# Kernel tuning notes

Measured on AMD Instinct MI355X. Metric: run time of the kernel, lower is better.

Reference implementation:

```python
import jax, jax.numpy as jnp
import numpy as np

B_SZ, LATENT, HIDDEN, T_STEPS = 512, 256, 512, 8
RTOL, ATOL = 1e-3, 1e-4
MAX_STEPS = 12          # adaptive sub-steps per output segment
SAFETY, MIN_FAC, MAX_FAC = 0.9, 0.2, 10.0

# Dormand-Prince 5(4) Butcher tableau (same as torchdiffeq's dopri5)
_C = [0.0, 0.2, 0.3, 0.8, 8.0 / 9.0, 1.0, 1.0]
_A = [
    [],
    [0.2],
    [3 / 40, 9 / 40],
    [44 / 45, -56 / 15, 32 / 9],
    [19372 / 6561, -25360 / 2187, 64448 / 6561, -212 / 729],
    [9017 / 3168, -355 / 33, 46732 / 5247, 49 / 176, -5103 / 18656],
    [35 / 384, 0.0, 500 / 1113, 125 / 192, -2187 / 6784, 11 / 84],
]
_B5 = [35 / 384, 0.0, 500 / 1113, 125 / 192, -2187 / 6784, 11 / 84, 0.0]
_B4 = [5179 / 57600, 0.0, 7571 / 16695, 393 / 640, -92097 / 339200, 187 / 2100, 1 / 40]


def _ode_rhs(p, t, z):
    # dz/dt = MLP([z, t]); t is a traced scalar
    b = z.shape[0]
    zt = jnp.concatenate([z, jnp.broadcast_to(t, (b, 1)).astype(z.dtype)], axis=1)
    h = jax.nn.relu(zt @ p['W1'] + p['b1'])
    h = jax.nn.relu(h @ p['W2'] + p['b2'])
    h = jax.nn.relu(h @ p['W3'] + p['b3'])
    return h @ p['W4'] + p['b4']


def _dopri5_step(p, t, z, dt):
    ks = []
    for i in range(7):
        zi = z
        for j, aij in enumerate(_A[i]):
            if aij != 0.0:
                zi = zi + (dt * aij) * ks[j]
        ks.append(_ode_rhs(p, t + _C[i] * dt, zi))
    z5 = z
    err = jnp.zeros_like(z)
    for i in range(7):
        if _B5[i] != 0.0:
            z5 = z5 + (dt * _B5[i]) * ks[i]
        d = _B5[i] - _B4[i]
        if d != 0.0:
            err = err + (dt * d) * ks[i]
    return z5, err


def _integrate(p, z0, t_grid):
    # adaptive dopri5 from t_grid[0] to each subsequent time, bounded work via scan
    def segment(carry, ts):
        z, dt = carry
        t0, t1 = ts[0], ts[1]

        def step(c, _):
            z, t, dt = c
            remaining = t1 - t
            active = remaining > 1e-10
            dt_try = jnp.minimum(dt, remaining)
            z5, err = _dopri5_step(p, t, z, dt_try)
            scale = ATOL + RTOL * jnp.maximum(jnp.abs(z), jnp.abs(z5))
            err_norm = jnp.sqrt(jnp.mean((err / scale) ** 2))
            accept = err_norm <= 1.0
            factor = jnp.clip(SAFETY * jnp.maximum(err_norm, 1e-9) ** -0.2, MIN_FAC, MAX_FAC)
            ok = jnp.logical_and(active, accept)
            z_n = jnp.where(ok, z5, z)
            t_n = jnp.where(ok, t + dt_try, t)
            dt_n = jnp.where(active, dt_try * factor, dt)
            return (z_n, t_n, dt_n), None

        (z, _, dt), _ = jax.lax.scan(step, (z, t0, dt), None, length=MAX_STEPS)
        return (z, dt), z

    dt0 = (t_grid[1] - t_grid[0]) * 0.1
    segs = jnp.stack([t_grid[:-1], t_grid[1:]], axis=1)  # [T-1, 2]
    (_, _), z_rest = jax.lax.scan(segment, (z0, dt0), segs)
    return jnp.concatenate([z0[None], z_rest], axis=0)  # [T, B, D]


def _pose_head(p, z):
    # z: [B, T, D]; dropout is identity in eval mode
    h = jax.nn.relu(z @ p['P1'] + p['pb1'])
    h = jax.nn.relu(h @ p['P2'] + p['pb2'])
    h = jax.nn.relu(h @ p['P3'] + p['pb3'])
    pose = h @ p['P4'] + p['pb4']  # [B, T, 7]
    pos, quat = pose[..., :3], pose[..., 3:]
    quat = quat / jnp.maximum(jnp.linalg.norm(quat, axis=-1, keepdims=True), 1e-12)
    return jnp.concatenate([pos, quat], axis=-1)


def setup_inputs() -> dict:
    key = jax.random.key(0)
    ks = jax.random.split(key, 12)
    n = jax.random.normal
    return {
        'z0': n(ks[0], (B_SZ, LATENT), dtype=jnp.float32),
        'time_steps': jnp.arange(T_STEPS, dtype=jnp.float32) / (T_STEPS - 1),
        # ODEFunc params (init std 0.1, zero bias per source)
        'W1': 0.1 * n(ks[1], (LATENT + 1, HIDDEN), dtype=jnp.float32),
        'b1': jnp.zeros((HIDDEN,), jnp.float32),
        'W2': 0.1 * n(ks[2], (HIDDEN, HIDDEN), dtype=jnp.float32),
        'b2': jnp.zeros((HIDDEN,), jnp.float32),
        'W3': 0.1 * n(ks[3], (HIDDEN, HIDDEN), dtype=jnp.float32),
        'b3': jnp.zeros((HIDDEN,), jnp.float32),
        'W4': 0.1 * n(ks[4], (HIDDEN, LATENT), dtype=jnp.float32),
        'b4': jnp.zeros((LATENT,), jnp.float32),
        # Pose head params
        'P1': 0.0625 * n(ks[5], (LATENT, 512), dtype=jnp.float32),
        'pb1': jnp.zeros((512,), jnp.float32),
        'P2': 0.0442 * n(ks[6], (512, 256), dtype=jnp.float32),
        'pb2': jnp.zeros((256,), jnp.float32),
        'P3': 0.0625 * n(ks[7], (256, 128), dtype=jnp.float32),
        'pb3': jnp.zeros((128,), jnp.float32),
        'P4': 0.01 * n(ks[8], (128, 7), dtype=jnp.float32),
        'pb4': jnp.zeros((7,), jnp.float32),
    }


def reference(z0, time_steps, W1, b1, W2, b2, W3, b3, W4, b4,
              P1, pb1, P2, pb2, P3, pb3, P4, pb4):
    p = dict(W1=W1, b1=b1, W2=W2, b2=b2, W3=W3, b3=b3, W4=W4, b4=b4,
             P1=P1, pb1=pb1, P2=P2, pb2=pb2, P3=P3, pb3=pb3, P4=P4, pb4=pb4)
    z_traj = _integrate(p, z0, time_steps)          # [T, B, D]
    z_traj = jnp.transpose(z_traj, (1, 0, 2))        # [B, T, D]
    poses = _pose_head(p, z_traj)                    # [B, T, 7]
    return poses
```

## Files before the change

### kernel.cpp

```cpp
#include <hip/hip_runtime.h>
#include <hip/hip_bf16.h>
#include <hip/hip_fp16.h>
#include <hip/hip_cooperative_groups.h>

namespace cg = cooperative_groups;

typedef unsigned short us16;
typedef unsigned int uu32;
typedef _Float16 h2v __attribute__((ext_vector_type(2)));

__constant__ float c_A[7][6] = {
  {0.f,0.f,0.f,0.f,0.f,0.f},
  {0.2f,0.f,0.f,0.f,0.f,0.f},
  {(float)(3.0/40.0),(float)(9.0/40.0),0.f,0.f,0.f,0.f},
  {(float)(44.0/45.0),(float)(-56.0/15.0),(float)(32.0/9.0),0.f,0.f,0.f},
  {(float)(19372.0/6561.0),(float)(-25360.0/2187.0),(float)(64448.0/6561.0),(float)(-212.0/729.0),0.f,0.f},
  {(float)(9017.0/3168.0),(float)(-355.0/33.0),(float)(46732.0/5247.0),(float)(49.0/176.0),(float)(-5103.0/18656.0),0.f},
  {(float)(35.0/384.0),0.f,(float)(500.0/1113.0),(float)(125.0/192.0),(float)(-2187.0/6784.0),(float)(11.0/84.0)}
};
__constant__ float c_C[7]  = {0.f,0.2f,0.3f,0.8f,(float)(8.0/9.0),1.f,1.f};
__constant__ float c_B5[7] = {(float)(35.0/384.0),0.f,(float)(500.0/1113.0),(float)(125.0/192.0),
                              (float)(-2187.0/6784.0),(float)(11.0/84.0),0.f};
__constant__ float c_D[7]  = {
  (float)(35.0/384.0 - 5179.0/57600.0), 0.f,
  (float)(500.0/1113.0 - 7571.0/16695.0),
  (float)(125.0/192.0 - 393.0/640.0),
  (float)(-2187.0/6784.0 + 92097.0/339200.0),
  (float)(11.0/84.0 - 187.0/2100.0),
  (float)(0.0 - 1.0/40.0)
};

#define P1N (128*512)
#define P2N (256*512)
#define P3N (256*512)
#define P4N (256*256)
#define PTOT (P1N+P2N+P3N+P4N)

struct Params {
  const void* z0; const void* tgrid;
  const void* W1; const void* b1; const void* W2; const void* b2;
  const void* W3; const void* b3; const void* W4; const void* b4;
  const void* P1; const void* pb1; const void* P2; const void* pb2;
  const void* P3; const void* pb3; const void* P4; const void* pb4;
  void* out; float* slots;
  const uu32* whBase;
  int useF16;
};

__device__ __forceinline__ float bflo(uu32 w){ return __uint_as_float(w << 16); }
__device__ __forceinline__ float bfhi(uu32 w){ return __uint_as_float(w & 0xffff0000u); }
__device__ __forceinline__ float ldbf(const us16* p, int i){
  return __uint_as_float(((uu32)p[i]) << 16);
}
__device__ __forceinline__ void f4a(float4 q, float* o){ o[0]=q.x; o[1]=q.y; o[2]=q.z; o[3]=q.w; }

__device__ __forceinline__ float fdot2(uu32 a, uu32 b, float c){
#if __has_builtin(__builtin_amdgcn_fdot2)
  return __builtin_amdgcn_fdot2(__builtin_bit_cast(h2v,a), __builtin_bit_cast(h2v,b), c, false);
#else
  __half2 ah = __builtin_bit_cast(__half2,a), bh = __builtin_bit_cast(__half2,b);
  c = fmaf(__low2float(ah), __low2float(bh), c);
  return fmaf(__high2float(ah), __high2float(bh), c);
#endif
}

template<bool BF16> struct IO;
template<> struct IO<true>{
  static __device__ __forceinline__ float ld(const void* p, int i){
    return __uint_as_float(((uu32)((const us16*)p)[i]) << 16);
  }
  static __device__ __forceinline__ float2 ldPair(const void* p, int i){
    uu32 w = ((const uu32*)p)[i];
    return make_float2(bflo(w), bfhi(w));
  }
  static __device__ __forceinline__ float4 ldQuad(const void* p, int i){
    uint2 w = ((const uint2*)p)[i];
    return make_float4(bflo(w.x), bfhi(w.x), bflo(w.y), bfhi(w.y));
  }
  static __device__ __forceinline__ void st(void* p, int i, float v){
    ((__hip_bfloat16*)p)[i] = __float2bfloat16(v);
  }
};
template<> struct IO<false>{
  static __device__ __forceinline__ float ld(const void* p, int i){ return ((const float*)p)[i]; }
  static __device__ __forceinline__ float2 ldPair(const void* p, int i){ return ((const float2*)p)[i]; }
  static __device__ __forceinline__ float4 ldQuad(const void* p, int i){ return ((const float4*)p)[i]; }
  static __device__ __forceinline__ void st(void* p, int i, float v){ ((float*)p)[i] = v; }
};

template<bool BF16, bool F16W, int K, bool ADDT>
__device__ __forceinline__ void layer512d(const us16* inb, const uu32* WP, const void* Wnat,
    const void* B, float ts, const float4 wt4, us16* outb, float* part, int tid)
{
  const int u = tid & 127, q = tid >> 7;
  constexpr int KH = K >> 4;
  float a[16];
  #pragma unroll
  for (int j=0;j<16;++j) a[j]=0.f;

  if constexpr (F16W){
    const uint4* Wb = (const uint4*)WP + (q*KH)*128 + u;
    const uu32* x0 = (const uu32*)inb + q*KH;
    #pragma unroll 4
    for (int kp = 0; kp < KH; ++kp){
      uint4 wq = Wb[kp*128];
      uu32 xv0 = x0[kp];
      uu32 xv1 = x0[(K>>1) + kp];
      uu32 xv2 = x0[2*(K>>1) + kp];
      uu32 xv3 = x0[3*(K>>1) + kp];
      a[0] = fdot2(xv0, wq.x, a[0]);  a[1] = fdot2(xv0, wq.y, a[1]);
      a[2] = fdot2(xv0, wq.z, a[2]);  a[3] = fdot2(xv0, wq.w, a[3]);
      a[4] = fdot2(xv1, wq.x, a[4]);  a[5] = fdot2(xv1, wq.y, a[5]);
      a[6] = fdot2(xv1, wq.z, a[6]);  a[7] = fdot2(xv1, wq.w, a[7]);
      a[8] = fdot2(xv2, wq.x, a[8]);  a[9] = fdot2(xv2, wq.y, a[9]);
      a[10]= fdot2(xv2, wq.z, a[10]); a[11]= fdot2(xv2, wq.w, a[11]);
      a[12]= fdot2(xv3, wq.x, a[12]); a[13]= fdot2(xv3, wq.y, a[13]);
      a[14]= fdot2(xv3, wq.z, a[14]); a[15]= fdot2(xv3, wq.w, a[15]);
    }
  } else {
    const int k0 = q*(K>>3);
    const __half* xh = (const __half*)inb;
    #pragma unroll 2
    for (int k = 0; k < (K>>3); ++k){
      float w[4];
      f4a(IO<BF16>::ldQuad(Wnat, (k0+k)*128 + u), w);
      #pragma unroll
      for (int r=0;r<4;++r){
        float xv = __half2float(xh[r*K + k0 + k]);
        #pragma unroll
        for (int c=0;c<4;++c) a[r*4+c] = fmaf(xv, w[c], a[r*4+c]);
      }
    }
  }

  if (ADDT && q == 0){
    float wt[4]; f4a(wt4, wt);
    #pragma unroll
    for (int r=0;r<4;++r)
      #pragma unroll
      for (int c=0;c<4;++c)
        a[r*4+c] += ts*wt[c];
  }

  float* p0 = part + ((q & 3) << 11) + (u << 2);
  if (q < 4){
    #pragma unroll
    for (int r=0;r<4;++r)
      *(float4*)(p0 + r*512) = make_float4(a[r*4],a[r*4+1],a[r*4+2],a[r*4+3]);
  }
  __syncthreads();
  if (q >= 4){
    #pragma unroll
    for (int r=0;r<4;++r){
      float4 t4 = *(float4*)(p0 + r*512);
      t4.x += a[r*4]; t4.y += a[r*4+1]; t4.z += a[r*4+2]; t4.w += a[r*4+3];
      *(float4*)(p0 + r*512) = t4;
    }
  }
  __syncthreads();
  #pragma unroll
  for (int p=0;p<2;++p){
    const int idx = p*1024 + tid;
    const int r = idx >> 9, n = idx & 511;
    float s = IO<BF16>::ld(B, n);
    #pragma unroll
    for (int s4=0;s4<4;++s4) s += part[(s4<<11) + (r<<9) + n];
    s = fmaxf(s, 0.f);
    ((__half*)outb)[r*512 + n] = __float2half(s);
  }
  __syncthreads();
}

template<bool BF16, bool F16W>
__device__ __forceinline__ void layerW4d(const us16* inb, const uu32* WP, const void* Wnat,
    const void* B, float* kbO, float* part, int tid)
{
  const int u = tid & 127, q = tid >> 7;
  float a[8];
  #pragma unroll
  for (int j=0;j<8;++j) a[j]=0.f;

  if constexpr (F16W){
    const uint2* Wb = (const uint2*)WP + (q*32)*128 + u;
    const uu32* x0 = (const uu32*)inb + q*32;
    #pragma unroll 4
    for (int kp = 0; kp < 32; ++kp){
      uint2 wq = Wb[kp*128];
      uu32 xv0 = x0[kp];
      uu32 xv1 = x0[256 + kp];
      uu32 xv2 = x0[512 + kp];
      uu32 xv3 = x0[768 + kp];
      a[0] = fdot2(xv0, wq.x, a[0]);  a[1] = fdot2(xv0, wq.y, a[1]);
      a[2] = fdot2(xv1, wq.x, a[2]);  a[3] = fdot2(xv1, wq.y, a[3]);
      a[4] = fdot2(xv2, wq.x, a[4]);  a[5] = fdot2(xv2, wq.y, a[5]);
      a[6] = fdot2(xv3, wq.x, a[6]);  a[7] = fdot2(xv3, wq.y, a[7]);
    }
  } else {
    const int k0 = q*64;
    const __half* xh = (const __half*)inb;
    #pragma unroll 2
    for (int k = 0; k < 64; ++k){
      float2 w = IO<BF16>::ldPair(Wnat, (k0+k)*128 + u);
      #pragma unroll
      for (int r=0;r<4;++r){
        float xv = __half2float(xh[r*512 + k0 + k]);
        a[r*2]   = fmaf(xv, w.x, a[r*2]);
        a[r*2+1] = fmaf(xv, w.y, a[r*2+1]);
      }
    }
  }

  float* p0 = part + ((q & 3) << 10) + (u << 1);
  if (q < 4){
    #pragma unroll
    for (int r=0;r<4;++r)
      *(float2*)(p0 + r*256) = make_float2(a[r*2], a[r*2+1]);
  }
  __syncthreads();
  if (q >= 4){
    #pragma unroll
    for (int r=0;r<4;++r){
      float2 t2 = *(float2*)(p0 + r*256);
      t2.x += a[r*2]; t2.y += a[r*2+1];
      *(float2*)(p0 + r*256) = t2;
    }
  }
  __syncthreads();
  {
    const int r = tid >> 8, n = tid & 255;
    float s = IO<BF16>::ld(B, n);
    #pragma unroll
    for (int s4=0;s4<4;++s4) s += part[(s4<<10) + (r<<8) + n];
    kbO[r*256 + n] = s;
  }
  __syncthreads();
}

template<bool BF16, bool F16W>
__device__ void runAll(const Params& P, float* sm, int tid, int blk, cg::grid_group grid)
{
  us16* zih = (us16*)sm;
  us16* hh  = (us16*)(sm + 512);
  float* kb  = sm + 1536;
  float* red = sm + 8704;
  float* part= sm + 8720;
  us16* traj = (us16*)(sm + 16912);
  float* pA = sm;
  float* pB = sm + 8192;
  float* pC = sm + 12288;
  float* pO = sm + 14336;

  const uu32* wp1 = P.whBase;
  const uu32* wp2 = wp1 + P1N;
  const uu32* wp3 = wp2 + P2N;
  const uu32* wp4 = wp3 + P3N;

  const int uu = tid & 127;
  const float4 wt1 = IO<BF16>::ldQuad(P.W1, 32768 + uu);

  if (blk == 0 && tid < 96)
    __hip_atomic_store(&P.slots[tid], 0.0f, __ATOMIC_RELAXED, __HIP_MEMORY_SCOPE_AGENT);

  const int g0 = blk*4;
  const int row = tid >> 8, n = tid & 255;
  float zz = IO<BF16>::ld(P.z0, (g0+row)*256 + n);
  traj[tid] = (us16)(__bfloat16_as_ushort(__float2bfloat16(zz)));
  grid.sync();

  float dt = (IO<BF16>::ld(P.tgrid,1) - IO<BF16>::ld(P.tgrid,0)) * 0.1f;
  int scount = 0;

  for (int seg = 0; seg < 7; ++seg){
    const float t1s = IO<BF16>::ld(P.tgrid, seg+1);
    float t = IO<BF16>::ld(P.tgrid, seg);
    bool fsal = false;

    for (int it = 0; it < 12; ++it){
      float remaining = t1s - t;
      if (!(remaining > 1e-10f)) break;
      float dt_try = fminf(dt, remaining);

      const int i0 = fsal ? 1 : 0;
      for (int i = i0; i < 7; ++i){
        float v = zz;
        #pragma unroll
        for (int j = 0; j < 6; ++j)
          if (j < i) v += (dt_try * c_A[i][j]) * kb[j*1024 + tid];
        ((__half*)zih)[row*256 + n] = __float2half(v);
        __syncthreads();
        const float ts = t + c_C[i]*dt_try;
        layer512d<BF16,F16W,256,true >(zih, wp1, P.W1, P.b1, ts,  wt1, hh, part, tid);
        layer512d<BF16,F16W,512,false>(hh,  wp2, P.W2, P.b2, 0.f, wt1, hh, part, tid);
        layer512d<BF16,F16W,512,false>(hh,  wp3, P.W3, P.b3, 0.f, wt1, hh, part, tid);
        layerW4d<BF16,F16W>(hh, wp4, P.W4, P.b4, kb + i*1024, part, tid);
      }

      float sq, z5v;
      {
        float zv = zz;
        z5v = zv; float ev = 0.f;
        #pragma unroll
        for (int i = 0; i < 7; ++i){
          float kv = kb[i*1024 + tid];
          if (c_B5[i] != 0.f) z5v += (dt_try*c_B5[i]) * kv;
          if (c_D[i]  != 0.f) ev  += (dt_try*c_D[i])  * kv;
        }
        float sc = 1e-4f + 1e-3f * fmaxf(fabsf(zv), fabsf(z5v));
        float e = ev / sc;
        sq = e*e;
      }
      #pragma unroll
      for (int o = 32; o > 0; o >>= 1) sq += __shfl_down(sq, o, 64);
      if ((tid & 63) == 0) red[tid >> 6] = sq;
      __syncthreads();
      if (tid == 0){
        float s = 0.f;
        #pragma unroll
        for (int w = 0; w < 16; ++w) s += red[w];
        atomicAdd(&P.slots[scount], s);
      }
      grid.sync();
      float tot = __hip_atomic_load(&P.slots[scount], __ATOMIC_RELAXED, __HIP_MEMORY_SCOPE_AGENT);
      scount++;

      float err_norm = sqrtf(tot * (1.0f/131072.0f));
      float factor = fminf(fmaxf(0.9f * powf(fmaxf(err_norm, 1e-9f), -0.2f), 0.2f), 10.0f);
      if (err_norm <= 1.0f){
        zz = z5v;
        t = t + dt_try;
        kb[tid] = kb[6*1024 + tid];
      }
      fsal = true;
      dt = dt_try * factor;
      __syncthreads();
    }

    traj[(seg+1)*1024 + tid] = (us16)(__bfloat16_as_ushort(__float2bfloat16(zz)));
    __syncthreads();
  }

  const int q2 = tid >> 8, u2 = tid & 255;
  for (int pp = 0; pp < 2; ++pp){
    const us16* zin = traj + pp*4096;
    {
      float a[8];
      #pragma unroll
      for (int j=0;j<8;++j) a[j]=0.f;
      #pragma unroll 2
      for (int k = 0; k < 256; ++k){
        float2 wv = IO<BF16>::ldPair(P.P1, (k << 8) + u2);
        #pragma unroll
        for (int rr=0;rr<4;++rr){
          float xv = ldbf(zin + (q2*4+rr)*256, k);
          a[rr*2]   = fmaf(xv, wv.x, a[rr*2]);
          a[rr*2+1] = fmaf(xv, wv.y, a[rr*2+1]);
        }
      }
      float b0 = IO<BF16>::ld(P.pb1, 2*u2), b1 = IO<BF16>::ld(P.pb1, 2*u2+1);
      #pragma unroll
      for (int rr=0;rr<4;++rr)
        *(float2*)(pA + (q2*4+rr)*512 + 2*u2) =
          make_float2(fmaxf(a[rr*2]+b0, 0.f), fmaxf(a[rr*2+1]+b1, 0.f));
    }
    __syncthreads();
    {
      float a[4] = {0.f,0.f,0.f,0.f};
      #pragma unroll 4
      for (int k = 0; k < 512; ++k){
        float wv = IO<BF16>::ld(P.P2, (k << 8) + u2);
        #pragma unroll
        for (int rr=0;rr<4;++rr)
          a[rr] = fmaf(pA[(q2*4+rr)*512 + k], wv, a[rr]);
      }
      float b = IO<BF16>::ld(P.pb2, u2);
      #pragma unroll
      for (int rr=0;rr<4;++rr)
        pB[(q2*4+rr)*256 + u2] = fmaxf(a[rr]+b, 0.f);
    }
    __syncthreads();
    if (u2 < 128){
      float a[4] = {0.f,0.f,0.f,0.f};
      #pragma unroll 4
      for (int k = 0; k < 256; ++k){
        float wv = IO<BF16>::ld(P.P3, (k << 7) + u2);
        #pragma unroll
        for (int rr=0;rr<4;++rr)
          a[rr] = fmaf(pB[(q2*4+rr)*256 + k], wv, a[rr]);
      }
      float b = IO<BF16>::ld(P.pb3, u2);
      #pragma unroll
      for (int rr=0;rr<4;++rr)
        pC[(q2*4+rr)*128 + u2] = fmaxf(a[rr]+b, 0.f);
    }
    __syncthreads();
    if (u2 < 28){
      int rr = u2 / 7, c = u2 - rr*7;
      int ll = q2*4 + rr;
      float a = 0.f;
      const float* hx = pC + ll*128;
      #pragma unroll 8
      for (int k = 0; k < 128; ++k) a = fmaf(hx[k], IO<BF16>::ld(P.P4, k*7 + c), a);
      pO[ll*7 + c] = a + IO<BF16>::ld(P.pb4, c);
    }
    __syncthreads();
    if (u2 < 4){
      int ll = q2*4 + u2;
      int gl = pp*16 + ll;
      int tt = gl >> 2, r = gl & 3, b = g0 + r;
      const float* po = pO + ll*7;
      float qa = po[3], qb = po[4], qc = po[5], qd = po[6];
      float nn = fmaxf(sqrtf(qa*qa + qb*qb + qc*qc + qd*qd), 1e-12f);
      int ob = (b*8 + tt)*7;
      IO<BF16>::st(P.out, ob+0, po[0]);
      IO<BF16>::st(P.out, ob+1, po[1]);
      IO<BF16>::st(P.out, ob+2, po[2]);
      IO<BF16>::st(P.out, ob+3, qa/nn);
      IO<BF16>::st(P.out, ob+4, qb/nn);
      IO<BF16>::st(P.out, ob+5, qc/nn);
      IO<BF16>::st(P.out, ob+6, qd/nn);
    }
    __syncthreads();
  }
}

__global__ void convert_weights(const void* tgrid,
    const void* W1, const void* W2, const void* W3, const void* W4, uu32* out)
{
  const us16* tg = (const us16*)tgrid;
  float v7 = __uint_as_float(((uu32)tg[7]) << 16);
  float v1 = __uint_as_float(((uu32)tg[1]) << 16);
  bool isbf16 = (v7 > 0.99f && v7 < 1.01f && v1 > 0.05f && v1 < 0.25f);

  int i = blockIdx.x*blockDim.x + threadIdx.x;
  const int stride = gridDim.x*blockDim.x;
  for (; i < PTOT; i += stride){
    const void* src; int e, sh;
    if (i < P1N){ src = W1; e = i; sh = 9; }
    else if (i < P1N+P2N){ src = W2; e = i - P1N; sh = 9; }
    else if (i < P1N+P2N+P3N){ src = W3; e = i - (P1N+P2N); sh = 9; }
    else { src = W4; e = i - (P1N+P2N+P3N); sh = 8; }
    const int kp = e >> sh, c = e & ((1<<sh)-1), N = 1<<sh;
    float lo, hi;
    if (isbf16){
      lo = __uint_as_float(((uu32)((const us16*)src)[(2*kp)*N + c]) << 16);
      hi = __uint_as_float(((uu32)((const us16*)src)[(2*kp+1)*N + c]) << 16);
    } else {
      lo = ((const float*)src)[(2*kp)*N + c];
      hi = ((const float*)src)[(2*kp+1)*N + c];
    }
    __half hl = __float2half(lo), hh = __float2half(hi);
    out[i] = ((uu32)__builtin_bit_cast(us16, hh) << 16) | (uu32)__builtin_bit_cast(us16, hl);
  }
}

__global__ __launch_bounds__(1024, 4)
void ode_pose_kernel(Params P)
{
  __shared__ float sm[21008];
  cg::grid_group grid = cg::this_grid();
  int tid = threadIdx.x, blk = blockIdx.x;

  const us16* tg = (const us16*)P.tgrid;
  float v7 = __uint_as_float(((uu32)tg[7]) << 16);
  float v1 = __uint_as_float(((uu32)tg[1]) << 16);
  bool isbf16 = (v7 > 0.99f && v7 < 1.01f && v1 > 0.05f && v1 < 0.25f);

  if (isbf16){
    if (P.useF16) runAll<true, true >(P, sm, tid, blk, grid);
    else          runAll<true, false>(P, sm, tid, blk, grid);
  } else {
    if (P.useF16) runAll<false, true >(P, sm, tid, blk, grid);
    else          runAll<false, false>(P, sm, tid, blk, grid);
  }
}

extern "C" void kernel_launch(void* const* d_in, const int* in_sizes, int n_in,
                              void* d_out, int out_size, void* d_ws, size_t ws_size,
                              hipStream_t stream)
{
  (void)in_sizes; (void)n_in; (void)out_size;
  Params P;
  P.z0  = d_in[0];  P.tgrid = d_in[1];
  P.W1  = d_in[2];  P.b1  = d_in[3];
  P.W2  = d_in[4];  P.b2  = d_in[5];
  P.W3  = d_in[6];  P.b3  = d_in[7];
  P.W4  = d_in[8];  P.b4  = d_in[9];
  P.P1  = d_in[10]; P.pb1 = d_in[11];
  P.P2  = d_in[12]; P.pb2 = d_in[13];
  P.P3  = d_in[14]; P.pb3 = d_in[15];
  P.P4  = d_in[16]; P.pb4 = d_in[17];
  P.out = d_out;
  P.slots = (float*)d_ws;

  const size_t need = 1024 + (size_t)PTOT*4;
  P.useF16 = (ws_size >= need) ? 1 : 0;
  P.whBase = (const uu32*)((const char*)d_ws + 1024);

  if (P.useF16){
    hipLaunchKernelGGL(convert_weights, dim3(1024), dim3(256), 0, stream,
                       P.tgrid, P.W1, P.W2, P.W3, P.W4, (uu32*)((char*)d_ws + 1024));
  }

  void* args[] = { &P };
  hipLaunchCooperativeKernel((void*)ode_pose_kernel, dim3(128), dim3(1024), args, 0, stream);
}
```

Before: 3.217 ms.

## Halve rows per block and double the cooperative grid to 256 blocks

Each block now integrates 2 batch rows instead of 4, and the cooperative launch grows from 128 to 256 blocks. This spreads the sequential ODE work over more compute units and shrinks the per-block shared memory footprint. In exchange, each weight load is reused across only 2 rows instead of 4, so total weight traffic doubles, and more blocks join each grid-wide error reduction. Half the threads now sit idle in the elementwise stages.

```diff
diff --git a/kernel.cpp b/kernel.cpp
--- a/kernel.cpp
+++ b/kernel.cpp
@@ -94,9 +94,9 @@
 {
   const int u = tid & 127, q = tid >> 7;
   constexpr int KH = K >> 4;
-  float a[16];
+  float a[8];
   #pragma unroll
-  for (int j=0;j<16;++j) a[j]=0.f;
+  for (int j=0;j<8;++j) a[j]=0.f;
 
   if constexpr (F16W){
     const uint4* Wb = (const uint4*)WP + (q*KH)*128 + u;
@@ -106,16 +106,10 @@
       uint4 wq = Wb[kp*128];
       uu32 xv0 = x0[kp];
       uu32 xv1 = x0[(K>>1) + kp];
-      uu32 xv2 = x0[2*(K>>1) + kp];
-      uu32 xv3 = x0[3*(K>>1) + kp];
       a[0] = fdot2(xv0, wq.x, a[0]);  a[1] = fdot2(xv0, wq.y, a[1]);
       a[2] = fdot2(xv0, wq.z, a[2]);  a[3] = fdot2(xv0, wq.w, a[3]);
       a[4] = fdot2(xv1, wq.x, a[4]);  a[5] = fdot2(xv1, wq.y, a[5]);
       a[6] = fdot2(xv1, wq.z, a[6]);  a[7] = fdot2(xv1, wq.w, a[7]);
-      a[8] = fdot2(xv2, wq.x, a[8]);  a[9] = fdot2(xv2, wq.y, a[9]);
-      a[10]= fdot2(xv2, wq.z, a[10]); a[11]= fdot2(xv2, wq.w, a[11]);
-      a[12]= fdot2(xv3, wq.x, a[12]); a[13]= fdot2(xv3, wq.y, a[13]);
-      a[14]= fdot2(xv3, wq.z, a[14]); a[15]= fdot2(xv3, wq.w, a[15]);
     }
   } else {
     const int k0 = q*(K>>3);
@@ -125,7 +119,7 @@
       float w[4];
       f4a(IO<BF16>::ldQuad(Wnat, (k0+k)*128 + u), w);
       #pragma unroll
-      for (int r=0;r<4;++r){
+      for (int r=0;r<2;++r){
         float xv = __half2float(xh[r*K + k0 + k]);
         #pragma unroll
         for (int c=0;c<4;++c) a[r*4+c] = fmaf(xv, w[c], a[r*4+c]);
@@ -136,35 +130,33 @@
   if (ADDT && q == 0){
     float wt[4]; f4a(wt4, wt);
     #pragma unroll
-    for (int r=0;r<4;++r)
+    for (int r=0;r<2;++r)
       #pragma unroll
       for (int c=0;c<4;++c)
         a[r*4+c] += ts*wt[c];
   }
 
-  float* p0 = part + ((q & 3) << 11) + (u << 2);
+  float* p0 = part + ((q & 3) << 10) + (u << 2);
   if (q < 4){
     #pragma unroll
-    for (int r=0;r<4;++r)
+    for (int r=0;r<2;++r)
       *(float4*)(p0 + r*512) = make_float4(a[r*4],a[r*4+1],a[r*4+2],a[r*4+3]);
   }
   __syncthreads();
   if (q >= 4){
     #pragma unroll
-    for (int r=0;r<4;++r){
+    for (int r=0;r<2;++r){
       float4 t4 = *(float4*)(p0 + r*512);
       t4.x += a[r*4]; t4.y += a[r*4+1]; t4.z += a[r*4+2]; t4.w += a[r*4+3];
       *(float4*)(p0 + r*512) = t4;
     }
   }
   __syncthreads();
-  #pragma unroll
-  for (int p=0;p<2;++p){
-    const int idx = p*1024 + tid;
-    const int r = idx >> 9, n = idx & 511;
+  {
+    const int r = tid >> 9, n = tid & 511;
     float s = IO<BF16>::ld(B, n);
     #pragma unroll
-    for (int s4=0;s4<4;++s4) s += part[(s4<<11) + (r<<9) + n];
+    for (int s4=0;s4<4;++s4) s += part[(s4<<10) + (r<<9) + n];
     s = fmaxf(s, 0.f);
     ((__half*)outb)[r*512 + n] = __float2half(s);
   }
@@ -176,9 +168,9 @@
     const void* B, float* kbO, float* part, int tid)
 {
   const int u = tid & 127, q = tid >> 7;
-  float a[8];
+  float a[4];
   #pragma unroll
-  for (int j=0;j<8;++j) a[j]=0.f;
+  for (int j=0;j<4;++j) a[j]=0.f;
 
   if constexpr (F16W){
     const uint2* Wb = (const uint2*)WP + (q*32)*128 + u;
@@ -188,12 +180,8 @@
       uint2 wq = Wb[kp*128];
       uu32 xv0 = x0[kp];
       uu32 xv1 = x0[256 + kp];
-      uu32 xv2 = x0[512 + kp];
-      uu32 xv3 = x0[768 + kp];
       a[0] = fdot2(xv0, wq.x, a[0]);  a[1] = fdot2(xv0, wq.y, a[1]);
       a[2] = fdot2(xv1, wq.x, a[2]);  a[3] = fdot2(xv1, wq.y, a[3]);
-      a[4] = fdot2(xv2, wq.x, a[4]);  a[5] = fdot2(xv2, wq.y, a[5]);
-      a[6] = fdot2(xv3, wq.x, a[6]);  a[7] = fdot2(xv3, wq.y, a[7]);
     }
   } else {
     const int k0 = q*64;
@@ -202,7 +190,7 @@
     for (int k = 0; k < 64; ++k){
       float2 w = IO<BF16>::ldPair(Wnat, (k0+k)*128 + u);
       #pragma unroll
-      for (int r=0;r<4;++r){
+      for (int r=0;r<2;++r){
         float xv = __half2float(xh[r*512 + k0 + k]);
         a[r*2]   = fmaf(xv, w.x, a[r*2]);
         a[r*2+1] = fmaf(xv, w.y, a[r*2+1]);
@@ -210,27 +198,27 @@
     }
   }
 
-  float* p0 = part + ((q & 3) << 10) + (u << 1);
+  float* p0 = part + ((q & 3) << 9) + (u << 1);
   if (q < 4){
     #pragma unroll
-    for (int r=0;r<4;++r)
+    for (int r=0;r<2;++r)
       *(float2*)(p0 + r*256) = make_float2(a[r*2], a[r*2+1]);
   }
   __syncthreads();
   if (q >= 4){
     #pragma unroll
-    for (int r=0;r<4;++r){
+    for (int r=0;r<2;++r){
       float2 t2 = *(float2*)(p0 + r*256);
       t2.x += a[r*2]; t2.y += a[r*2+1];
       *(float2*)(p0 + r*256) = t2;
     }
   }
   __syncthreads();
-  {
+  if (tid < 512){
     const int r = tid >> 8, n = tid & 255;
     float s = IO<BF16>::ld(B, n);
     #pragma unroll
-    for (int s4=0;s4<4;++s4) s += part[(s4<<10) + (r<<8) + n];
+    for (int s4=0;s4<4;++s4) s += part[(s4<<9) + (r<<8) + n];
     kbO[r*256 + n] = s;
   }
   __syncthreads();
@@ -240,11 +228,11 @@
 __device__ void runAll(const Params& P, float* sm, int tid, int blk, cg::grid_group grid)
 {
   us16* zih = (us16*)sm;
-  us16* hh  = (us16*)(sm + 512);
-  float* kb  = sm + 1536;
-  float* red = sm + 8704;
-  float* part= sm + 8720;
-  us16* traj = (us16*)(sm + 16912);
+  us16* hh  = (us16*)(sm + 256);
+  float* kb  = sm + 768;
+  float* red = sm + 4352;
+  float* part= sm + 4368;
+  us16* traj = (us16*)(sm + 14448);
   float* pA = sm;
   float* pB = sm + 8192;
   float* pC = sm + 12288;
@@ -261,10 +249,13 @@
   if (blk == 0 && tid < 96)
     __hip_atomic_store(&P.slots[tid], 0.0f, __ATOMIC_RELAXED, __HIP_MEMORY_SCOPE_AGENT);
 
-  const int g0 = blk*4;
+  const int g0 = blk*2;
   const int row = tid >> 8, n = tid & 255;
-  float zz = IO<BF16>::ld(P.z0, (g0+row)*256 + n);
-  traj[tid] = (us16)(__bfloat16_as_ushort(__float2bfloat16(zz)));
+  float zz = 0.f;
+  if (tid < 512){
+    zz = IO<BF16>::ld(P.z0, (g0+row)*256 + n);
+    traj[tid] = (us16)(__bfloat16_as_ushort(__float2bfloat16(zz)));
+  }
   grid.sync();
 
   float dt = (IO<BF16>::ld(P.tgrid,1) - IO<BF16>::ld(P.tgrid,0)) * 0.1f;
@@ -282,26 +273,28 @@
 
       const int i0 = fsal ? 1 : 0;
       for (int i = i0; i < 7; ++i){
-        float v = zz;
-        #pragma unroll
-        for (int j = 0; j < 6; ++j)
-          if (j < i) v += (dt_try * c_A[i][j]) * kb[j*1024 + tid];
-        ((__half*)zih)[row*256 + n] = __float2half(v);
+        if (tid < 512){
+          float v = zz;
+          #pragma unroll
+          for (int j = 0; j < 6; ++j)
+            if (j < i) v += (dt_try * c_A[i][j]) * kb[j*512 + tid];
+          ((__half*)zih)[tid] = __float2half(v);
+        }
         __syncthreads();
         const float ts = t + c_C[i]*dt_try;
         layer512d<BF16,F16W,256,true >(zih, wp1, P.W1, P.b1, ts,  wt1, hh, part, tid);
         layer512d<BF16,F16W,512,false>(hh,  wp2, P.W2, P.b2, 0.f, wt1, hh, part, tid);
         layer512d<BF16,F16W,512,false>(hh,  wp3, P.W3, P.b3, 0.f, wt1, hh, part, tid);
-        layerW4d<BF16,F16W>(hh, wp4, P.W4, P.b4, kb + i*1024, part, tid);
-      }
-
-      float sq, z5v;
-      {
+        layerW4d<BF16,F16W>(hh, wp4, P.W4, P.b4, kb + i*512, part, tid);
+      }
+
+      float sq = 0.f, z5v = 0.f;
+      if (tid < 512){
         float zv = zz;
         z5v = zv; float ev = 0.f;
         #pragma unroll
         for (int i = 0; i < 7; ++i){
-          float kv = kb[i*1024 + tid];
+          float kv = kb[i*512 + tid];
           if (c_B5[i] != 0.f) z5v += (dt_try*c_B5[i]) * kv;
           if (c_D[i]  != 0.f) ev  += (dt_try*c_D[i])  * kv;
         }
@@ -326,22 +319,25 @@
       float err_norm = sqrtf(tot * (1.0f/131072.0f));
       float factor = fminf(fmaxf(0.9f * powf(fmaxf(err_norm, 1e-9f), -0.2f), 0.2f), 10.0f);
       if (err_norm <= 1.0f){
-        zz = z5v;
+        if (tid < 512){
+          zz = z5v;
+          kb[tid] = kb[6*512 + tid];
+        }
         t = t + dt_try;
-        kb[tid] = kb[6*1024 + tid];
       }
       fsal = true;
       dt = dt_try * factor;
       __syncthreads();
     }
 
-    traj[(seg+1)*1024 + tid] = (us16)(__bfloat16_as_ushort(__float2bfloat16(zz)));
+    if (tid < 512)
+      traj[(seg+1)*512 + tid] = (us16)(__bfloat16_as_ushort(__float2bfloat16(zz)));
     __syncthreads();
   }
 
   const int q2 = tid >> 8, u2 = tid & 255;
-  for (int pp = 0; pp < 2; ++pp){
-    const us16* zin = traj + pp*4096;
+  {
+    const us16* zin = traj;
     {
       float a[8];
       #pragma unroll
@@ -405,8 +401,7 @@
     __syncthreads();
     if (u2 < 4){
       int ll = q2*4 + u2;
-      int gl = pp*16 + ll;
-      int tt = gl >> 2, r = gl & 3, b = g0 + r;
+      int tt = ll >> 1, r = ll & 1, b = g0 + r;
       const float* po = pO + ll*7;
       float qa = po[3], qb = po[4], qc = po[5], qd = po[6];
       float nn = fmaxf(sqrtf(qa*qa + qb*qb + qc*qc + qd*qd), 1e-12f);
@@ -456,7 +451,7 @@
 __global__ __launch_bounds__(1024, 4)
 void ode_pose_kernel(Params P)
 {
-  __shared__ float sm[21008];
+  __shared__ float sm[16496];
   cg::grid_group grid = cg::this_grid();
   int tid = threadIdx.x, blk = blockIdx.x;
 
@@ -502,5 +497,5 @@
   }
 
   void* args[] = { &P };
-  hipLaunchCooperativeKernel((void*)ode_pose_kernel, dim3(128), dim3(1024), args, 0, stream);
-}
+  hipLaunchCooperativeKernel((void*)ode_pose_kernel, dim3(256), dim3(1024), args, 0, stream);
+}
```

After: 2.707 ms. -15.9%, faster.
